# Optimization experiments

Hardware: AMD Instinct MI355X
Metric: run time of the kernel (lower is better)

The kernel has to match this reference:

```python
import jax, jax.numpy as jnp
import numpy as np

B, D, P, K, H = 8192, 64, 4, 16, 5
IN = D * P  # 256
NEG_SLOPE = 0.2
EPS = 1e-6  # GaussianNLLLoss var clamp


def setup_inputs() -> dict:
    key = jax.random.key(0)
    ks = jax.random.split(key, 13)
    s1 = 1.0 / np.sqrt(IN)
    s2 = 1.0 / np.sqrt(H + IN)
    return {
        "x_values": jax.random.normal(ks[0], (B, D), jnp.float32),
        "x_inputs": jax.random.normal(ks[1], (B, D, IN), jnp.float32),
        "targets": 0.1 * jax.random.normal(ks[2], (D, K, K - 1), jnp.float32),
        "W1": s1 * jax.random.normal(ks[3], (K, D, H, IN), jnp.float32),
        "b1": s1 * jax.random.normal(ks[4], (D, K, H), jnp.float32),
        "Wh": s2 * jax.random.normal(ks[5], (K, D, H), jnp.float32),
        "Wx": s2 * jax.random.normal(ks[6], (K, D, IN), jnp.float32),
        "b2": s2 * jax.random.normal(ks[7], (D, K), jnp.float32),
        "sW1": s1 * jax.random.normal(ks[8], (K, D, H, IN), jnp.float32),
        "sb1": s1 * jax.random.normal(ks[9], (D, K, H), jnp.float32),
        "sWh": s2 * jax.random.normal(ks[10], (K, D, H), jnp.float32),
        "sWx": s2 * jax.random.normal(ks[11], (K, D, IN), jnp.float32),
        "sb2": s2 * jax.random.normal(ks[12], (D, K), jnp.float32),
    }


def _grouped_mlp(x, W1, b1, Wh, Wx, b2):
    # x: (B, d, in); one tiny net per (k, j): Linear(in->H) + LeakyReLU,
    # then final Linear on concat([hidden, x]) (NO trailing activation; torch code uses net[-2]).
    h = jax.nn.leaky_relu(jnp.einsum('bji,kjhi->bjkh', x, W1) + b1, NEG_SLOPE)  # (B,d,K,H)
    out = (jnp.einsum('bjkh,kjh->bjk', h, Wh)
           + jnp.einsum('bji,kji->bjk', x, Wx)
           + b2)  # (B,d,K), out_dim=1 squeezed
    return out


def _target_weights(targets):
    # base[j,k,:] = [0, (targets*tril(-1))[j,k,:]] + eye(K)[k]
    tril = jnp.tril(jnp.ones((K, K - 1), jnp.float32), -1)  # (K, K-1)
    base = jnp.concatenate(
        [jnp.zeros((D, K, 1), targets.dtype), targets * tril], axis=2
    ) + jnp.eye(K, dtype=targets.dtype)  # (D, K, K)
    row_mask = jnp.tril(jnp.ones((K, K), jnp.float32))  # row k keeps cols 0..k
    logits = jnp.where(row_mask.astype(bool), base, -1e30)
    w = jax.nn.softmax(logits, axis=-1) * row_mask  # (D, K, K)
    return w


def reference(x_values, x_inputs, targets, W1, b1, Wh, Wx, b2,
              sW1, sb1, sWh, sWx, sb2):
    mean = _grouped_mlp(x_inputs, W1, b1, Wh, Wx, b2)      # (B,d,K)
    shared = _grouped_mlp(x_inputs, sW1, sb1, sWh, sWx, sb2)
    var = jnp.maximum((10.0 * jax.nn.sigmoid(shared)) ** 2, EPS)
    # GaussianNLLLoss(reduction='none'), full=False
    nll_node = 0.5 * (jnp.log(var) + (x_values[:, :, None] - mean) ** 2 / var)  # (B,d,K)
    w = _target_weights(targets)  # (d, K, K) row-masked softmax weights
    # nll[b,i] = sum_j sum_{k<=i} nll_node[b,j,k] * w[j,i,k]
    nll = jnp.einsum('bjk,jik->bi', nll_node, w)  # (B, K)
    return nll
```

## Files before the change

kernel.cpp:

```cpp
#include <hip/hip_runtime.h>

typedef float f32x4 __attribute__((ext_vector_type(4)));
typedef short bf16x8 __attribute__((ext_vector_type(8)));

#define B_TOT 8192
#define D_ 64
#define K_ 16
#define H_ 5
#define IN_ 256

__device__ __forceinline__ unsigned short f2bf(float f){
  unsigned int u = __float_as_uint(f);
  u += 0x7fffu + ((u >> 16) & 1u);
  return (unsigned short)(u >> 16);
}

__global__ void pack_weights_kernel(const float* __restrict__ W1,
                                    const float* __restrict__ Wx,
                                    const float* __restrict__ sW1,
                                    const float* __restrict__ sWx,
                                    unsigned short* __restrict__ Wpack){
  int j = blockIdx.x;
  int r = blockIdx.y;
  int c = threadIdx.x;
  const float* src;
  if (r < 80)      { int k = r/5, h = r%5;            src = W1  + (((k*D_ + j)*H_ + h)*IN_); }
  else if (r < 96) { int k = r-80;                    src = Wx  + ((k*D_ + j)*IN_); }
  else if (r < 176){ int rr = r-96; int k=rr/5,h=rr%5; src = sW1 + (((k*D_ + j)*H_ + h)*IN_); }
  else             { int k = r-176;                   src = sWx + ((k*D_ + j)*IN_); }
  Wpack[((j*192 + r) << 8) + c] = f2bf(src[c]);
}

__global__ void compute_w_kernel(const float* __restrict__ targets, float* __restrict__ wout){
  int j = blockIdx.x;
  int i = threadIdx.x;
  if (i >= K_) return;
  float base[K_];
  base[0] = (i == 0) ? 1.f : 0.f;
  for (int c = 1; c <= i; ++c)
    base[c] = targets[(j*K_ + i)*(K_-1) + (c-1)] + ((c == i) ? 1.f : 0.f);
  float mx = base[0];
  for (int c = 1; c <= i; ++c) mx = fmaxf(mx, base[c]);
  float e[K_]; float s = 0.f;
  for (int c = 0; c <= i; ++c){ e[c] = expf(base[c] - mx); s += e[c]; }
  float inv = 1.f / s;
  for (int c = 0; c < K_; ++c)
    wout[(j*K_ + i)*K_ + c] = (c <= i) ? e[c]*inv : 0.f;
}

__global__ __launch_bounds__(256, 2)
void main_kernel(const float* __restrict__ x_values,
                 const float* __restrict__ x_inputs,
                 const unsigned short* __restrict__ Wpack,
                 const float* __restrict__ wsm,
                 const float* __restrict__ b1, const float* __restrict__ Wh, const float* __restrict__ b2,
                 const float* __restrict__ sb1, const float* __restrict__ sWh, const float* __restrict__ sb2,
                 float* __restrict__ partial){
  __shared__ __align__(16) char sm[65536];
  float* G    = (float*)sm;
  float* nn   = (float*)(sm + 50432);
  float* w_s  = (float*)(sm + 54784);
  float* xv_s = (float*)(sm + 55808);

  const int t    = threadIdx.x;
  const int jg   = blockIdx.x;
  const int b0   = blockIdx.y * 64;
  const int lane = t & 63;
  const int wv   = t >> 6;
  const int q    = wv;
  const int r    = t & 63;

  float accnll[4] = {0.f, 0.f, 0.f, 0.f};

  for (int jj = 0; jj < 4; ++jj){
    const int j = jg*4 + jj;
    f32x4 acc[4][3];
    #pragma unroll
    for (int m = 0; m < 4; ++m)
      #pragma unroll
      for (int n = 0; n < 3; ++n) acc[m][n] = (f32x4){0.f,0.f,0.f,0.f};

    #pragma unroll
    for (int kc = 0; kc < 2; ++kc){
      {
        const int cb = t & 15, r0 = t >> 4;
        #pragma unroll
        for (int p = 0; p < 4; ++p){
          const int row = p*16 + r0;
          const float* src = x_inputs + (((size_t)(b0 + row)*D_ + j) << 8) + kc*128 + cb*8;
          f32x4 v0 = *(const f32x4*)(src);
          f32x4 v1 = *(const f32x4*)(src + 4);
          bf16x8 o;
          o[0]=f2bf(v0[0]); o[1]=f2bf(v0[1]); o[2]=f2bf(v0[2]); o[3]=f2bf(v0[3]);
          o[4]=f2bf(v1[0]); o[5]=f2bf(v1[1]); o[6]=f2bf(v1[2]); o[7]=f2bf(v1[3]);
          *(bf16x8*)(sm + row*256 + ((cb*16) ^ ((row & 7) << 4))) = o;
        }
      }
      #pragma unroll
      for (int c2 = 0; c2 < 12; ++c2){
        const int idx = c2*256 + t;
        const int n = idx >> 4, cb = idx & 15;
        const unsigned short* src = Wpack + (((size_t)j*192 + n) << 8) + kc*128 + cb*8;
        bf16x8 v = *(const bf16x8*)src;
        *(bf16x8*)(sm + 16384 + n*256 + ((cb*16) ^ ((n & 7) << 4))) = v;
      }
      __syncthreads();
      #pragma unroll
      for (int kk = 0; kk < 4; ++kk){
        const int colb = kk*64 + ((lane >> 4) << 4);
        bf16x8 a[4], bfr[3];
        #pragma unroll
        for (int m = 0; m < 4; ++m){
          const int row = m*16 + (lane & 15);
          a[m] = *(const bf16x8*)(sm + row*256 + (colb ^ ((row & 7) << 4)));
        }
        #pragma unroll
        for (int n = 0; n < 3; ++n){
          const int row = wv*48 + n*16 + (lane & 15);
          bfr[n] = *(const bf16x8*)(sm + 16384 + row*256 + (colb ^ ((row & 7) << 4)));
        }
        #pragma unroll
        for (int m = 0; m < 4; ++m)
          #pragma unroll
          for (int n = 0; n < 3; ++n)
            acc[m][n] = __builtin_amdgcn_mfma_f32_16x16x32_bf16(a[m], bfr[n], acc[m][n], 0, 0, 0);
      }
      __syncthreads();
    }
    #pragma unroll
    for (int m = 0; m < 4; ++m){
      const int rbase = m*16 + ((lane >> 4) << 2);
      #pragma unroll
      for (int n = 0; n < 3; ++n){
        const int col = wv*48 + n*16 + (lane & 15);
        #pragma unroll
        for (int e = 0; e < 4; ++e)
          G[(rbase + e)*197 + col] = acc[m][n][e];
      }
    }
    w_s[t] = wsm[(j << 8) + t];
    if (t < 64) xv_s[t] = x_values[(size_t)(b0 + t)*D_ + j];
    __syncthreads();
    {
      const float xv = xv_s[r];
      #pragma unroll
      for (int kk = 0; kk < 4; ++kk){
        const int k = q*4 + kk;
        float mean = b2[j*K_ + k] + G[r*197 + 80 + k];
        #pragma unroll
        for (int h = 0; h < H_; ++h){
          float v = G[r*197 + k*H_ + h] + b1[(j*K_ + k)*H_ + h];
          v = (v > 0.f) ? v : 0.2f*v;
          mean += v * Wh[(k*D_ + j)*H_ + h];
        }
        float sh = sb2[j*K_ + k] + G[r*197 + 176 + k];
        #pragma unroll
        for (int h = 0; h < H_; ++h){
          float v = G[r*197 + 96 + k*H_ + h] + sb1[(j*K_ + k)*H_ + h];
          v = (v > 0.f) ? v : 0.2f*v;
          sh += v * sWh[(k*D_ + j)*H_ + h];
        }
        float sg  = 10.f / (1.f + expf(-sh));
        float var = fmaxf(sg*sg, 1e-6f);
        float d   = xv - mean;
        nn[r*17 + k] = 0.5f*(logf(var) + d*d/var);
      }
    }
    __syncthreads();
    #pragma unroll
    for (int ii = 0; ii < 4; ++ii){
      const int i = q*4 + ii;
      float s = 0.f;
      #pragma unroll
      for (int k = 0; k < K_; ++k) s += nn[r*17 + k] * w_s[i*K_ + k];
      accnll[ii] += s;
    }
    __syncthreads();
  }
  #pragma unroll
  for (int ii = 0; ii < 4; ++ii)
    partial[((size_t)jg*B_TOT + b0 + r)*K_ + q*4 + ii] = accnll[ii];
}

__global__ void reduce_kernel(const float* __restrict__ partial, float* __restrict__ out){
  int idx = blockIdx.x*256 + threadIdx.x;
  float s = 0.f;
  #pragma unroll
  for (int g = 0; g < 16; ++g) s += partial[(size_t)g*(B_TOT*K_) + idx];
  out[idx] = s;
}

extern "C" void kernel_launch(void* const* d_in, const int* in_sizes, int n_in,
                              void* d_out, int out_size, void* d_ws, size_t ws_size,
                              hipStream_t stream){
  const float* x_values = (const float*)d_in[0];
  const float* x_inputs = (const float*)d_in[1];
  const float* targets  = (const float*)d_in[2];
  const float* W1  = (const float*)d_in[3];
  const float* b1  = (const float*)d_in[4];
  const float* Wh  = (const float*)d_in[5];
  const float* Wx  = (const float*)d_in[6];
  const float* b2  = (const float*)d_in[7];
  const float* sW1 = (const float*)d_in[8];
  const float* sb1 = (const float*)d_in[9];
  const float* sWh = (const float*)d_in[10];
  const float* sWx = (const float*)d_in[11];
  const float* sb2 = (const float*)d_in[12];
  (void)in_sizes; (void)n_in; (void)out_size; (void)ws_size;

  char* ws = (char*)d_ws;
  unsigned short* Wpack = (unsigned short*)ws;
  float* wsm     = (float*)(ws + 6291456);
  float* partial = (float*)(ws + 6356992);
  float* out = (float*)d_out;

  pack_weights_kernel<<<dim3(64, 192), 256, 0, stream>>>(W1, Wx, sW1, sWx, Wpack);
  compute_w_kernel<<<dim3(64), 64, 0, stream>>>(targets, wsm);
  main_kernel<<<dim3(16, 128), 256, 0, stream>>>(x_values, x_inputs, Wpack, wsm,
                                                 b1, Wh, b2, sb1, sWh, sb2, partial);
  reduce_kernel<<<dim3(512), 256, 0, stream>>>(partial, out);
}
```

Before: 204.8 us.

## Software-pipeline main kernel with register-prefetched fragments and MFMA second layer

Weights are repacked into an MFMA-fragment-friendly layout so B fragments load straight from global into registers, double-buffered across the 8 (column, K-chunk) stages. The next stage's x_inputs tile is prefetched into registers while the current MFMAs run. The hidden-to-output layer (Wh/sWh) now runs as a small bf16 MFMA with bias and LeakyReLU fused into the epilogue. The final weighted reduction uses lane shuffles instead of an LDS round trip. This raises register pressure, adds extra bf16 rounding of hidden activations, and adds two more small pack kernels.

```diff
diff --git a/kernel.cpp b/kernel.cpp
--- a/kernel.cpp
+++ b/kernel.cpp
@@ -2,6 +2,7 @@
 
 typedef float f32x4 __attribute__((ext_vector_type(4)));
 typedef short bf16x8 __attribute__((ext_vector_type(8)));
+typedef unsigned int u32x4 __attribute__((ext_vector_type(4)));
 
 #define B_TOT 8192
 #define D_ 64
@@ -15,20 +16,44 @@
   return (unsigned short)(u >> 16);
 }
 
-__global__ void pack_weights_kernel(const float* __restrict__ W1,
-                                    const float* __restrict__ Wx,
-                                    const float* __restrict__ sW1,
-                                    const float* __restrict__ sWx,
-                                    unsigned short* __restrict__ Wpack){
-  int j = blockIdx.x;
-  int r = blockIdx.y;
-  int c = threadIdx.x;
+__global__ void pack_weights2_kernel(const float* __restrict__ W1,
+                                     const float* __restrict__ Wx,
+                                     const float* __restrict__ sW1,
+                                     const float* __restrict__ sWx,
+                                     unsigned short* __restrict__ Wpack2){
+  int j = blockIdx.x, r = blockIdx.y, c = threadIdx.x;
   const float* src;
-  if (r < 80)      { int k = r/5, h = r%5;            src = W1  + (((k*D_ + j)*H_ + h)*IN_); }
-  else if (r < 96) { int k = r-80;                    src = Wx  + ((k*D_ + j)*IN_); }
+  if (r < 80)      { int k = r/5, h = r%5;             src = W1  + (((k*D_ + j)*H_ + h)*IN_); }
+  else if (r < 96) { int k = r-80;                     src = Wx  + ((k*D_ + j)*IN_); }
   else if (r < 176){ int rr = r-96; int k=rr/5,h=rr%5; src = sW1 + (((k*D_ + j)*H_ + h)*IN_); }
-  else             { int k = r-176;                   src = sWx + ((k*D_ + j)*IN_); }
-  Wpack[((j*192 + r) << 8) + c] = f2bf(src[c]);
+  else             { int k = r-176;                    src = sWx + ((k*D_ + j)*IN_); }
+  int kk = c >> 5, ks = (c >> 3) & 3, e = c & 7;
+  Wpack2[((((size_t)j*8 + kk)*192 + r)*4 + ks)*8 + e] = f2bf(src[c]);
+}
+
+__global__ void pack_b1_kernel(const float* __restrict__ b1, const float* __restrict__ sb1,
+                               float* __restrict__ b1pack){
+  int j = blockIdx.x, r = threadIdx.x;
+  float v = 0.f;
+  if (r < 80) v = b1[j*80 + r];
+  else if (r >= 96 && r < 176) v = sb1[j*80 + (r-96)];
+  b1pack[j*192 + r] = v;
+}
+
+__global__ void pack_b2t_kernel(const float* __restrict__ Wh, const float* __restrict__ sWh,
+                                unsigned short* __restrict__ B2pack){
+  int j = blockIdx.x, t = threadIdx.x;
+  u32x4 z = {0,0,0,0};
+  *(u32x4*)((char*)B2pack + (size_t)j*8192 + t*32)      = z;
+  *(u32x4*)((char*)B2pack + (size_t)j*8192 + t*32 + 16) = z;
+  __syncthreads();
+  if (t < 160){
+    int half = t / 80, idx = t % 80, k = idx/5, h = idx%5;
+    int row = half*16 + k, col = idx;
+    const float* W = half ? sWh : Wh;
+    unsigned short v = f2bf(W[((size_t)k*D_ + j)*H_ + h]);
+    *(unsigned short*)((char*)B2pack + (size_t)j*8192 + row*208 + col*2) = v;
+  }
 }
 
 __global__ void compute_w_kernel(const float* __restrict__ targets, float* __restrict__ wout){
@@ -51,135 +76,202 @@
 __global__ __launch_bounds__(256, 2)
 void main_kernel(const float* __restrict__ x_values,
                  const float* __restrict__ x_inputs,
-                 const unsigned short* __restrict__ Wpack,
+                 const unsigned short* __restrict__ Wpack2,
                  const float* __restrict__ wsm,
-                 const float* __restrict__ b1, const float* __restrict__ Wh, const float* __restrict__ b2,
-                 const float* __restrict__ sb1, const float* __restrict__ sWh, const float* __restrict__ sb2,
+                 const float* __restrict__ b1pack,
+                 const unsigned short* __restrict__ B2pack,
+                 const float* __restrict__ b2, const float* __restrict__ sb2,
                  float* __restrict__ partial){
-  __shared__ __align__(16) char sm[65536];
-  float* G    = (float*)sm;
-  float* nn   = (float*)(sm + 50432);
-  float* w_s  = (float*)(sm + 54784);
-  float* xv_s = (float*)(sm + 55808);
-
-  const int t    = threadIdx.x;
-  const int jg   = blockIdx.x;
-  const int b0   = blockIdx.y * 64;
-  const int lane = t & 63;
-  const int wv   = t >> 6;
-  const int q    = wv;
-  const int r    = t & 63;
-
-  float accnll[4] = {0.f, 0.f, 0.f, 0.f};
-
-  for (int jj = 0; jj < 4; ++jj){
+  __shared__ __align__(16) char sm[61440];
+  unsigned short* G = (unsigned short*)(sm + 16384);
+  float* Gx  = (float*)(sm + 41984);
+  float* Gsx = (float*)(sm + 47104);
+  char*  B2T = sm + 52224;
+  float* w_l = (float*)(sm + 60416);
+
+  const int t   = threadIdx.x;
+  const int lane = t & 63, wv = t >> 6;
+  const int l15 = lane & 15, lg = lane >> 4;
+  const int jg = blockIdx.x, b0 = blockIdx.y * 64;
+
+  f32x4 acc1[4][3];
+  f32x4 acc3 = {0.f,0.f,0.f,0.f};
+  bf16x8 bfr[2][12];
+  f32x4 aA[8];
+  u32x4 b2tR0, b2tR1;
+
+  b2tR0 = *(const u32x4*)((const char*)B2pack + (size_t)(jg*4)*8192 + t*32);
+  b2tR1 = *(const u32x4*)((const char*)B2pack + (size_t)(jg*4)*8192 + t*32 + 16);
+  {
+    const int jN = jg*4;
+    const float* ap = x_inputs + ((size_t)(b0 + (t>>4))*D_ + jN)*IN_ + (t&15)*8;
+    #pragma unroll
+    for (int p = 0; p < 4; ++p){
+      aA[p*2]   = *(const f32x4*)(ap + (size_t)p*16*D_*IN_);
+      aA[p*2+1] = *(const f32x4*)(ap + (size_t)p*16*D_*IN_ + 4);
+    }
+    #pragma unroll
+    for (int kkl = 0; kkl < 4; ++kkl)
+      #pragma unroll
+      for (int n = 0; n < 3; ++n){
+        const int o = wv*48 + n*16 + l15;
+        bfr[0][kkl*3+n] = *(const bf16x8*)(Wpack2 + ((((size_t)jN*8 + kkl)*192 + o)*4 + lg)*8);
+      }
+    #pragma unroll
+    for (int p = 0; p < 4; ++p){
+      const int row = p*16 + (t>>4);
+      bf16x8 o;
+      o[0]=f2bf(aA[p*2][0]);   o[1]=f2bf(aA[p*2][1]);   o[2]=f2bf(aA[p*2][2]);   o[3]=f2bf(aA[p*2][3]);
+      o[4]=f2bf(aA[p*2+1][0]); o[5]=f2bf(aA[p*2+1][1]); o[6]=f2bf(aA[p*2+1][2]); o[7]=f2bf(aA[p*2+1][3]);
+      *(bf16x8*)(sm + row*256 + (((t&15)*16) ^ ((row & 7) << 4))) = o;
+    }
+  }
+  __syncthreads();
+
+  #pragma unroll
+  for (int s = 0; s < 8; ++s){
+    const int jj = s >> 1, kc = s & 1, cur = s & 1;
     const int j = jg*4 + jj;
-    f32x4 acc[4][3];
+
+    if (kc == 0){
+      *(u32x4*)(B2T + t*32)      = b2tR0;
+      *(u32x4*)(B2T + t*32 + 16) = b2tR1;
+      w_l[t] = wsm[(j << 8) + t];
+      #pragma unroll
+      for (int m = 0; m < 4; ++m)
+        #pragma unroll
+        for (int n = 0; n < 3; ++n) acc1[m][n] = (f32x4){0.f,0.f,0.f,0.f};
+    }
+
+    if (s < 7){
+      const int sn = s+1, jjN = sn>>1, kcN = sn&1, jN = jg*4 + jjN;
+      const float* ap = x_inputs + ((size_t)(b0 + (t>>4))*D_ + jN)*IN_ + kcN*128 + (t&15)*8;
+      #pragma unroll
+      for (int p = 0; p < 4; ++p){
+        aA[p*2]   = *(const f32x4*)(ap + (size_t)p*16*D_*IN_);
+        aA[p*2+1] = *(const f32x4*)(ap + (size_t)p*16*D_*IN_ + 4);
+      }
+      #pragma unroll
+      for (int kkl = 0; kkl < 4; ++kkl)
+        #pragma unroll
+        for (int n = 0; n < 3; ++n){
+          const int o = wv*48 + n*16 + l15;
+          bfr[sn&1][kkl*3+n] = *(const bf16x8*)(Wpack2 + ((((size_t)jN*8 + kcN*4 + kkl)*192 + o)*4 + lg)*8);
+        }
+      if (kcN == 0){
+        b2tR0 = *(const u32x4*)((const char*)B2pack + (size_t)jN*8192 + t*32);
+        b2tR1 = *(const u32x4*)((const char*)B2pack + (size_t)jN*8192 + t*32 + 16);
+      }
+    }
+
     #pragma unroll
-    for (int m = 0; m < 4; ++m)
-      #pragma unroll
-      for (int n = 0; n < 3; ++n) acc[m][n] = (f32x4){0.f,0.f,0.f,0.f};
-
-    #pragma unroll
-    for (int kc = 0; kc < 2; ++kc){
-      {
-        const int cb = t & 15, r0 = t >> 4;
-        #pragma unroll
-        for (int p = 0; p < 4; ++p){
-          const int row = p*16 + r0;
-          const float* src = x_inputs + (((size_t)(b0 + row)*D_ + j) << 8) + kc*128 + cb*8;
-          f32x4 v0 = *(const f32x4*)(src);
-          f32x4 v1 = *(const f32x4*)(src + 4);
-          bf16x8 o;
-          o[0]=f2bf(v0[0]); o[1]=f2bf(v0[1]); o[2]=f2bf(v0[2]); o[3]=f2bf(v0[3]);
-          o[4]=f2bf(v1[0]); o[5]=f2bf(v1[1]); o[6]=f2bf(v1[2]); o[7]=f2bf(v1[3]);
-          *(bf16x8*)(sm + row*256 + ((cb*16) ^ ((row & 7) << 4))) = o;
+    for (int kkl = 0; kkl < 4; ++kkl){
+      bf16x8 af[4];
+      #pragma unroll
+      for (int m = 0; m < 4; ++m){
+        const int row = m*16 + l15;
+        af[m] = *(const bf16x8*)(sm + row*256 + ((kkl*64 + lg*16) ^ ((row & 7) << 4)));
+      }
+      #pragma unroll
+      for (int m = 0; m < 4; ++m)
+        #pragma unroll
+        for (int n = 0; n < 3; ++n)
+          acc1[m][n] = __builtin_amdgcn_mfma_f32_16x16x32_bf16(af[m], bfr[cur][kkl*3+n], acc1[m][n], 0, 0, 0);
+    }
+
+    __syncthreads();
+
+    if (s < 7){
+      #pragma unroll
+      for (int p = 0; p < 4; ++p){
+        const int row = p*16 + (t>>4);
+        bf16x8 o;
+        o[0]=f2bf(aA[p*2][0]);   o[1]=f2bf(aA[p*2][1]);   o[2]=f2bf(aA[p*2][2]);   o[3]=f2bf(aA[p*2][3]);
+        o[4]=f2bf(aA[p*2+1][0]); o[5]=f2bf(aA[p*2+1][1]); o[6]=f2bf(aA[p*2+1][2]); o[7]=f2bf(aA[p*2+1][3]);
+        *(bf16x8*)(sm + row*256 + (((t&15)*16) ^ ((row & 7) << 4))) = o;
+      }
+    }
+
+    if (kc == 1){
+      #pragma unroll
+      for (int n = 0; n < 3; ++n){
+        const int col = wv*48 + n*16 + l15;
+        const bool isx  = (col >= 80 && col < 96);
+        const bool issx = (col >= 176);
+        const float b1v = (isx || issx) ? 0.f : b1pack[j*192 + col];
+        #pragma unroll
+        for (int m = 0; m < 4; ++m){
+          const int row = m*16 + lg*4;
+          if (isx){
+            #pragma unroll
+            for (int e = 0; e < 4; ++e){
+              Gx[(row+e)*20 + (col-80)] = acc1[m][n][e];
+              G[(row+e)*200 + col] = 0;
+            }
+          } else if (issx){
+            #pragma unroll
+            for (int e = 0; e < 4; ++e){
+              Gsx[(row+e)*20 + (col-176)] = acc1[m][n][e];
+              G[(row+e)*200 + col] = 0;
+            }
+          } else {
+            #pragma unroll
+            for (int e = 0; e < 4; ++e){
+              float v = acc1[m][n][e] + b1v;
+              v = fmaxf(v, 0.2f*v);
+              G[(row+e)*200 + col] = f2bf(v);
+            }
+          }
         }
       }
-      #pragma unroll
-      for (int c2 = 0; c2 < 12; ++c2){
-        const int idx = c2*256 + t;
-        const int n = idx >> 4, cb = idx & 15;
-        const unsigned short* src = Wpack + (((size_t)j*192 + n) << 8) + kc*128 + cb*8;
-        bf16x8 v = *(const bf16x8*)src;
-        *(bf16x8*)(sm + 16384 + n*256 + ((cb*16) ^ ((n & 7) << 4))) = v;
-      }
       __syncthreads();
-      #pragma unroll
-      for (int kk = 0; kk < 4; ++kk){
-        const int colb = kk*64 + ((lane >> 4) << 4);
-        bf16x8 a[4], bfr[3];
-        #pragma unroll
-        for (int m = 0; m < 4; ++m){
-          const int row = m*16 + (lane & 15);
-          a[m] = *(const bf16x8*)(sm + row*256 + (colb ^ ((row & 7) << 4)));
+
+      const int brow = wv*16 + l15;
+      f32x4 accm = *(const f32x4*)(Gx  + brow*20 + lg*4) + *(const f32x4*)(b2  + j*16 + lg*4);
+      f32x4 accs = *(const f32x4*)(Gsx + brow*20 + lg*4) + *(const f32x4*)(sb2 + j*16 + lg*4);
+      #pragma unroll
+      for (int kk = 0; kk < 3; ++kk){
+        bf16x8 a0 = *(const bf16x8*)(B2T + l15*208      + kk*64 + lg*16);
+        bf16x8 a1 = *(const bf16x8*)(B2T + (16+l15)*208 + kk*64 + lg*16);
+        bf16x8 g0 = *(const bf16x8*)((char*)G + brow*400       + kk*64 + lg*16);
+        bf16x8 g1 = *(const bf16x8*)((char*)G + brow*400 + 192 + kk*64 + lg*16);
+        accm = __builtin_amdgcn_mfma_f32_16x16x32_bf16(a0, g0, accm, 0, 0, 0);
+        accs = __builtin_amdgcn_mfma_f32_16x16x32_bf16(a1, g1, accs, 0, 0, 0);
+      }
+
+      const float xv = x_values[(size_t)(b0 + brow)*D_ + j];
+      float nn4[4];
+      #pragma unroll
+      for (int e = 0; e < 4; ++e){
+        float mean = accm[e];
+        float shv  = accs[e];
+        float ex = __expf(-shv);
+        float sg = __fdividef(10.f, 1.f + ex);
+        float var = fmaxf(sg*sg, 1e-6f);
+        float d = xv - mean;
+        nn4[e] = 0.5f*(__logf(var) + __fdividef(d*d, var));
+      }
+
+      #pragma unroll
+      for (int g = 0; g < 4; ++g){
+        float v0 = nn4[0], v1 = nn4[1], v2 = nn4[2], v3 = nn4[3];
+        if (g){
+          v0 = __shfl_xor(v0, g<<4); v1 = __shfl_xor(v1, g<<4);
+          v2 = __shfl_xor(v2, g<<4); v3 = __shfl_xor(v3, g<<4);
         }
-        #pragma unroll
-        for (int n = 0; n < 3; ++n){
-          const int row = wv*48 + n*16 + (lane & 15);
-          bfr[n] = *(const bf16x8*)(sm + 16384 + row*256 + (colb ^ ((row & 7) << 4)));
+        const int kb = ((lg ^ g) << 2);
+        #pragma unroll
+        for (int q = 0; q < 4; ++q){
+          f32x4 wq = *(const f32x4*)(w_l + (lg*4+q)*16 + kb);
+          acc3[q] += wq[0]*v0 + wq[1]*v1 + wq[2]*v2 + wq[3]*v3;
         }
-        #pragma unroll
-        for (int m = 0; m < 4; ++m)
-          #pragma unroll
-          for (int n = 0; n < 3; ++n)
-            acc[m][n] = __builtin_amdgcn_mfma_f32_16x16x32_bf16(a[m], bfr[n], acc[m][n], 0, 0, 0);
-      }
-      __syncthreads();
-    }
-    #pragma unroll
-    for (int m = 0; m < 4; ++m){
-      const int rbase = m*16 + ((lane >> 4) << 2);
-      #pragma unroll
-      for (int n = 0; n < 3; ++n){
-        const int col = wv*48 + n*16 + (lane & 15);
-        #pragma unroll
-        for (int e = 0; e < 4; ++e)
-          G[(rbase + e)*197 + col] = acc[m][n][e];
-      }
-    }
-    w_s[t] = wsm[(j << 8) + t];
-    if (t < 64) xv_s[t] = x_values[(size_t)(b0 + t)*D_ + j];
-    __syncthreads();
-    {
-      const float xv = xv_s[r];
-      #pragma unroll
-      for (int kk = 0; kk < 4; ++kk){
-        const int k = q*4 + kk;
-        float mean = b2[j*K_ + k] + G[r*197 + 80 + k];
-        #pragma unroll
-        for (int h = 0; h < H_; ++h){
-          float v = G[r*197 + k*H_ + h] + b1[(j*K_ + k)*H_ + h];
-          v = (v > 0.f) ? v : 0.2f*v;
-          mean += v * Wh[(k*D_ + j)*H_ + h];
-        }
-        float sh = sb2[j*K_ + k] + G[r*197 + 176 + k];
-        #pragma unroll
-        for (int h = 0; h < H_; ++h){
-          float v = G[r*197 + 96 + k*H_ + h] + sb1[(j*K_ + k)*H_ + h];
-          v = (v > 0.f) ? v : 0.2f*v;
-          sh += v * sWh[(k*D_ + j)*H_ + h];
-        }
-        float sg  = 10.f / (1.f + expf(-sh));
-        float var = fmaxf(sg*sg, 1e-6f);
-        float d   = xv - mean;
-        nn[r*17 + k] = 0.5f*(logf(var) + d*d/var);
-      }
-    }
-    __syncthreads();
-    #pragma unroll
-    for (int ii = 0; ii < 4; ++ii){
-      const int i = q*4 + ii;
-      float s = 0.f;
-      #pragma unroll
-      for (int k = 0; k < K_; ++k) s += nn[r*17 + k] * w_s[i*K_ + k];
-      accnll[ii] += s;
-    }
+      }
+    }
+
     __syncthreads();
   }
-  #pragma unroll
-  for (int ii = 0; ii < 4; ++ii)
-    partial[((size_t)jg*B_TOT + b0 + r)*K_ + q*4 + ii] = accnll[ii];
+
+  *(f32x4*)(partial + ((size_t)jg*B_TOT + b0 + wv*16 + l15)*16 + lg*4) = acc3;
 }
 
 __global__ void reduce_kernel(const float* __restrict__ partial, float* __restrict__ out){
@@ -209,14 +301,18 @@
   (void)in_sizes; (void)n_in; (void)out_size; (void)ws_size;
 
   char* ws = (char*)d_ws;
-  unsigned short* Wpack = (unsigned short*)ws;
+  unsigned short* Wpack2 = (unsigned short*)ws;
   float* wsm     = (float*)(ws + 6291456);
-  float* partial = (float*)(ws + 6356992);
+  float* b1pack  = (float*)(ws + 6356992);
+  unsigned short* B2pack = (unsigned short*)(ws + 6406144);
+  float* partial = (float*)(ws + 6930432);
   float* out = (float*)d_out;
 
-  pack_weights_kernel<<<dim3(64, 192), 256, 0, stream>>>(W1, Wx, sW1, sWx, Wpack);
+  pack_weights2_kernel<<<dim3(64, 192), 256, 0, stream>>>(W1, Wx, sW1, sWx, Wpack2);
+  pack_b1_kernel<<<dim3(64), 192, 0, stream>>>(b1, sb1, b1pack);
+  pack_b2t_kernel<<<dim3(64), 256, 0, stream>>>(Wh, sWh, B2pack);
   compute_w_kernel<<<dim3(64), 64, 0, stream>>>(targets, wsm);
-  main_kernel<<<dim3(16, 128), 256, 0, stream>>>(x_values, x_inputs, Wpack, wsm,
-                                                 b1, Wh, b2, sb1, sWh, sb2, partial);
+  main_kernel<<<dim3(16, 128), 256, 0, stream>>>(x_values, x_inputs, Wpack2, wsm,
+                                                 b1pack, B2pack, b2, sb2, partial);
   reduce_kernel<<<dim3(512), 256, 0, stream>>>(partial, out);
 }
```

Result: slower. 329.2 us (+60.8%).
